# Kernel tuning notes

Hardware: AMD Instinct MI355X
Metric: run time of the kernel (lower is better)

The kernel has to match this reference:

```python
import jax, jax.numpy as jnp
import numpy as np

DIM = 1024
N_HIDDEN = 64
NUM_HEADS = 16
B, S = 4, 1024
# original torch code: scale = sqrt(n_hidden // num_heads) = sqrt(64 // 16) = 2.0
SCALE = float(np.sqrt(N_HIDDEN // NUM_HEADS))


def setup_inputs() -> dict:
    key = jax.random.key(0)
    ks = jax.random.split(key, 10)
    lim = 1.0 / np.sqrt(DIM)          # nn.Linear default init range
    lim_o = 1.0 / np.sqrt(N_HIDDEN * NUM_HEADS)
    u = lambda k, shape, l: jax.random.uniform(k, shape, jnp.float32, -l, l)
    x = jax.random.normal(ks[0], (B, S, DIM), jnp.float32)
    attn_mask = jax.random.randint(ks[1], (B, S, S), 0, 2).astype(jnp.int32)
    # stacked per-head projection weights: [H, dim, n_hidden]
    Wq = u(ks[2], (NUM_HEADS, DIM, N_HIDDEN), lim)
    bq = u(ks[3], (NUM_HEADS, N_HIDDEN), lim)
    Wk = u(ks[4], (NUM_HEADS, DIM, N_HIDDEN), lim)
    bk = u(ks[5], (NUM_HEADS, N_HIDDEN), lim)
    Wv = u(ks[6], (NUM_HEADS, DIM, N_HIDDEN), lim)
    bv = u(ks[7], (NUM_HEADS, N_HIDDEN), lim)
    Wo = u(ks[8], (NUM_HEADS * N_HIDDEN, DIM), lim_o)
    bo = u(ks[9], (DIM,), lim_o)
    return {"x": x, "attn_mask": attn_mask, "Wq": Wq, "bq": bq,
            "Wk": Wk, "bk": bk, "Wv": Wv, "bv": bv, "Wo": Wo, "bo": bo}


def reference(x, attn_mask, Wq, bq, Wk, bk, Wv, bv, Wo, bo):
    # batched QKV across all heads (replaces the per-head Python loop)
    Q = jnp.einsum('bsd,hde->bhse', x, Wq) + bq[None, :, None, :]
    K = jnp.einsum('bsd,hde->bhse', x, Wk) + bk[None, :, None, :]
    V = jnp.einsum('bsd,hde->bhse', x, Wv) + bv[None, :, None, :]
    scores = jnp.einsum('bhse,bhte->bhst', Q, K) / SCALE
    alpha = jax.nn.softmax(scores, axis=-1)
    # faithful to original: zero out masked entries AFTER softmax, no renorm
    alpha = jnp.where(attn_mask[:, None, :, :] == 0, 0.0, alpha)  # [B,H,S,S]
    out = jnp.einsum('bhst,bhte->bhse', alpha, V)                 # [B,H,S,E]
    # torch.cat over heads on last dim == reshape to [B,S,H*E] in head order
    concat = out.transpose(0, 2, 1, 3).reshape(B, S, NUM_HEADS * N_HIDDEN)
    attn_output = concat @ Wo + bo                                # [B,S,dim]
    return attn_output, alpha
```

## Files before the change

### kernel.cpp

```cpp
#include <hip/hip_runtime.h>
#include <stdint.h>

#define S_LEN 1024
#define DIM   1024
#define NHID  64
#define NHEAD 16
#define NB    4

typedef __bf16 bf16x8 __attribute__((ext_vector_type(8)));
typedef float  f32x4  __attribute__((ext_vector_type(4)));
typedef unsigned short u16;

__device__ __forceinline__ u16 f2b(float f) {
  unsigned u = __float_as_uint(f);
  u += 0x7FFFu + ((u >> 16) & 1u);
  return (u16)(u >> 16);
}

__device__ __forceinline__ f32x4 mfma16(bf16x8 a, bf16x8 b, f32x4 c) {
  return __builtin_amdgcn_mfma_f32_16x16x32_bf16(a, b, c, 0, 0, 0);
}

__global__ __launch_bounds__(256) void k_cvt_x(const float* __restrict__ x,
                                               u16* __restrict__ xb) {
  int i = blockIdx.x * 256 + threadIdx.x;
  float4 v = ((const float4*)x)[i];
  ushort4 o;
  o.x = f2b(v.x); o.y = f2b(v.y); o.z = f2b(v.z); o.w = f2b(v.w);
  ((ushort4*)xb)[i] = o;
}

__global__ __launch_bounds__(256) void k_maskbits(const int* __restrict__ mask,
                                                  uint32_t* __restrict__ bits) {
  int w = blockIdx.x * 256 + threadIdx.x;
  const int4* mp = (const int4*)mask + (size_t)w * 8;
  uint32_t v = 0;
#pragma unroll
  for (int i = 0; i < 8; ++i) {
    int4 m = mp[i];
    v |= (m.x != 0 ? 1u : 0u) << (i * 4 + 0);
    v |= (m.y != 0 ? 1u : 0u) << (i * 4 + 1);
    v |= (m.z != 0 ? 1u : 0u) << (i * 4 + 2);
    v |= (m.w != 0 ? 1u : 0u) << (i * 4 + 3);
  }
  bits[w] = v;
}

__global__ __launch_bounds__(256) void k_transpose(const float* __restrict__ in,
                                                   u16* __restrict__ out,
                                                   int R, int C) {
  const float* ip = in + (size_t)blockIdx.x * R * C;
  u16* op = out + (size_t)blockIdx.x * R * C;
  __shared__ float tile[32][65];
  int r0 = blockIdx.y * 32, c0 = blockIdx.z * 64;
  int t = threadIdx.x;
  {
    int col = t & 63, rr = t >> 6;
#pragma unroll
    for (int p = 0; p < 8; ++p) {
      int r = p * 4 + rr;
      tile[r][col] = ip[(size_t)(r0 + r) * C + c0 + col];
    }
  }
  __syncthreads();
  {
    int d = t & 31, er = t >> 5;
#pragma unroll
    for (int p = 0; p < 8; ++p) {
      int e = p * 8 + er;
      op[(size_t)(c0 + e) * R + r0 + d] = f2b(tile[d][e]);
    }
  }
}

__global__ __launch_bounds__(256) void k_qkv(const u16* __restrict__ xb,
                                             const u16* __restrict__ Wtb,
                                             const float* __restrict__ bq,
                                             const float* __restrict__ bk,
                                             const float* __restrict__ bv,
                                             u16* __restrict__ Qb,
                                             u16* __restrict__ Kb,
                                             u16* __restrict__ Vtb) {
  __shared__ __align__(16) char lds[32768];
  int t = threadIdx.x, w = t >> 6, lane = t & 63;
  int l15 = lane & 15, l4 = lane >> 4;
  int m0 = blockIdx.x * 128, n0 = blockIdx.y * 128, sel = blockIdx.z;
  const u16* Wh = Wtb + (size_t)sel * (NHEAD * NHID * DIM);
  int wr = w >> 1, wc = w & 1;

  f32x4 acc[4][4];
  const f32x4 fz = {0.f, 0.f, 0.f, 0.f};
#pragma unroll
  for (int i = 0; i < 4; ++i)
#pragma unroll
    for (int j = 0; j < 4; ++j) acc[i][j] = fz;

  for (int kk = 0; kk < 16; ++kk) {
    int k0 = kk * 64;
#pragma unroll
    for (int c = 0; c < 4; ++c) {
      int idx = c * 256 + t, r = idx >> 3, cb = idx & 7;
      int4 v = *(const int4*)(xb + (size_t)(m0 + r) * DIM + k0 + cb * 8);
      *(int4*)(lds + r * 128 + ((cb * 16) ^ ((r & 7) << 4))) = v;
    }
#pragma unroll
    for (int c = 0; c < 4; ++c) {
      int idx = c * 256 + t, r = idx >> 3, cb = idx & 7;
      int4 v = *(const int4*)(Wh + (size_t)(n0 + r) * DIM + k0 + cb * 8);
      *(int4*)(lds + 16384 + r * 128 + ((cb * 16) ^ ((r & 7) << 4))) = v;
    }
    __syncthreads();
    bf16x8 a[4][2], bb[4][2];
#pragma unroll
    for (int mf = 0; mf < 4; ++mf)
#pragma unroll
      for (int kc = 0; kc < 2; ++kc) {
        int row = wr * 64 + mf * 16 + l15;
        int kb = kc * 64 + l4 * 16;
        a[mf][kc] = *(const bf16x8*)(lds + row * 128 + (kb ^ ((row & 7) << 4)));
      }
#pragma unroll
    for (int nf = 0; nf < 4; ++nf)
#pragma unroll
      for (int kc = 0; kc < 2; ++kc) {
        int row = wc * 64 + nf * 16 + l15;
        int kb = kc * 64 + l4 * 16;
        bb[nf][kc] = *(const bf16x8*)(lds + 16384 + row * 128 + (kb ^ ((row & 7) << 4)));
      }
#pragma unroll
    for (int kc = 0; kc < 2; ++kc)
#pragma unroll
      for (int mf = 0; mf < 4; ++mf)
#pragma unroll
        for (int nf = 0; nf < 4; ++nf)
          acc[mf][nf] = mfma16(a[mf][kc], bb[nf][kc], acc[mf][nf]);
    __syncthreads();
  }

  const float* bias = (sel == 0) ? bq : (sel == 1) ? bk : bv;
  float postScale = (sel == 0) ? 0.5f : 1.0f;
#pragma unroll
  for (int nf = 0; nf < 4; ++nf) {
    int n = n0 + wc * 64 + nf * 16 + l15;
    int h = n >> 6, e = n & 63;
    float bv_ = bias[n];
#pragma unroll
    for (int mf = 0; mf < 4; ++mf) {
      int mrow0 = m0 + wr * 64 + mf * 16 + l4 * 4;
      int b_ = mrow0 >> 10, s0 = mrow0 & 1023;
      if (sel == 2) {
        ushort4 pk;
        pk.x = f2b(acc[mf][nf][0] + bv_);
        pk.y = f2b(acc[mf][nf][1] + bv_);
        pk.z = f2b(acc[mf][nf][2] + bv_);
        pk.w = f2b(acc[mf][nf][3] + bv_);
        *(ushort4*)(Vtb + ((size_t)(b_ * NHEAD + h) * NHID + e) * S_LEN + s0) = pk;
      } else {
        u16* dst = (sel == 0) ? Qb : Kb;
#pragma unroll
        for (int j = 0; j < 4; ++j)
          dst[((size_t)(b_ * NHEAD + h) * S_LEN + s0 + j) * NHID + e] =
              f2b((acc[mf][nf][j] + bv_) * postScale);
      }
    }
  }
}

__global__ __launch_bounds__(256, 4) void k_attn(const u16* __restrict__ Qb,
                                                 const u16* __restrict__ Kb,
                                                 const u16* __restrict__ Vtb,
                                                 const uint32_t* __restrict__ mbitsG,
                                                 float* __restrict__ alphaOut,
                                                 u16* __restrict__ Ob) {
  __shared__ __align__(16) char smem[19072];
  uint32_t* mbits = (uint32_t*)smem;
  float* redM = (float*)(smem + 2176);
  float* redS = (float*)(smem + 2432);
  char* chunkB = smem + 2688;
  int t = threadIdx.x, w = t >> 6, lane = t & 63;
  int l15 = lane & 15, l4 = lane >> 4;
  int q0 = blockIdx.x * 16;
  int bh = blockIdx.y, b = bh >> 4, hh = bh & 15;
  const u16* Qh = Qb + (size_t)bh * S_LEN * NHID;
  const u16* Kh = Kb + (size_t)bh * S_LEN * NHID;
  const u16* Vh = Vtb + (size_t)bh * NHID * S_LEN;
  int kbase = w * 256;

  uint2 mw2 = ((const uint2*)(mbitsG + ((size_t)b * S_LEN + q0) * 32))[t];

  bf16x8 aq[2];
#pragma unroll
  for (int ec = 0; ec < 2; ++ec)
    aq[ec] = *(const bf16x8*)(Qh + (size_t)(q0 + l15) * NHID + ec * 32 + l4 * 8);

  {
    int row = t >> 4, c0 = (t & 15) * 2;
    mbits[row * 33 + c0 + 0] = mw2.x;
    mbits[row * 33 + c0 + 1] = mw2.y;
  }

  f32x4 sc[16];
  const f32x4 fz = {0.f, 0.f, 0.f, 0.f};
#pragma unroll
  for (int kf = 0; kf < 16; ++kf) sc[kf] = fz;

#pragma unroll
  for (int kf = 0; kf < 16; ++kf) {
    int key = kbase + kf * 16 + l15;
    bf16x8 kb0 = *(const bf16x8*)(Kh + (size_t)key * NHID + l4 * 8);
    bf16x8 kb1 = *(const bf16x8*)(Kh + (size_t)key * NHID + 32 + l4 * 8);
    sc[kf] = mfma16(aq[0], kb0, sc[kf]);
    sc[kf] = mfma16(aq[1], kb1, sc[kf]);
  }

  float rm[4];
#pragma unroll
  for (int j = 0; j < 4; ++j) {
    float m = sc[0][j];
#pragma unroll
    for (int kf = 1; kf < 16; ++kf) m = fmaxf(m, sc[kf][j]);
    rm[j] = m;
  }
#pragma unroll
  for (int msk = 1; msk < 16; msk <<= 1)
#pragma unroll
    for (int j = 0; j < 4; ++j) rm[j] = fmaxf(rm[j], __shfl_xor(rm[j], msk));
  if (l15 == 0) {
#pragma unroll
    for (int j = 0; j < 4; ++j) redM[w * 16 + l4 * 4 + j] = rm[j];
  }
  __syncthreads();
  float Mx[4];
#pragma unroll
  for (int j = 0; j < 4; ++j) {
    int row = l4 * 4 + j;
    Mx[j] = fmaxf(fmaxf(redM[row], redM[16 + row]),
                  fmaxf(redM[32 + row], redM[48 + row]));
  }

  float ls[4] = {0.f, 0.f, 0.f, 0.f};
#pragma unroll
  for (int kf = 0; kf < 16; ++kf)
#pragma unroll
    for (int j = 0; j < 4; ++j) {
      float p = __expf(sc[kf][j] - Mx[j]);
      sc[kf][j] = p;
      ls[j] += p;
    }
#pragma unroll
  for (int msk = 1; msk < 16; msk <<= 1)
#pragma unroll
    for (int j = 0; j < 4; ++j) ls[j] += __shfl_xor(ls[j], msk);
  if (l15 == 0) {
#pragma unroll
    for (int j = 0; j < 4; ++j) redS[w * 16 + l4 * 4 + j] = ls[j];
  }
  __syncthreads();
  float inv[4];
#pragma unroll
  for (int j = 0; j < 4; ++j) {
    int row = l4 * 4 + j;
    inv[j] = 1.f / (redS[row] + redS[16 + row] + redS[32 + row] + redS[48 + row]);
  }

  float* abW = alphaOut + (size_t)bh * S_LEN * S_LEN;

  f32x4 o[4];
#pragma unroll
  for (int ef = 0; ef < 4; ++ef) o[ef] = fz;

  auto produce = [&](int c) {
    char* buf = chunkB + (w * 2 + (c & 1)) * 2048;
    int widxBase = w * 8 + c * 2;
#pragma unroll
    for (int f = 0; f < 4; ++f) {
      int kf = c * 4 + f;
      int keyg = kbase + kf * 16 + l15;
      int widx = widxBase + (f >> 1);
      int bitpos = ((f & 1) << 4) + l15;
#pragma unroll
      for (int j = 0; j < 4; ++j) {
        int row = l4 * 4 + j;
        uint32_t mwd = mbits[row * 33 + widx];
        float av = ((mwd >> bitpos) & 1u) ? sc[kf][j] * inv[j] : 0.f;
        __builtin_nontemporal_store(av, abW + (size_t)(q0 + row) * S_LEN + keyg);
        int klc = f * 16 + l15;
        *(u16*)(buf + row * 128 + ((2 * klc) ^ ((row & 7) << 4))) = f2b(av);
      }
    }
  };
  auto pv = [&](int c) {
    char* buf = chunkB + (w * 2 + (c & 1)) * 2048;
#pragma unroll
    for (int kc2 = 0; kc2 < 2; ++kc2) {
      int qrow = l15;
      bf16x8 pa = *(const bf16x8*)(buf + qrow * 128 +
                                   ((kc2 * 64 + l4 * 16) ^ ((qrow & 7) << 4)));
#pragma unroll
      for (int ef = 0; ef < 4; ++ef) {
        int e = ef * 16 + l15;
        bf16x8 vb = *(const bf16x8*)(Vh + (size_t)e * S_LEN + kbase + c * 64 +
                                     kc2 * 32 + l4 * 8);
        o[ef] = mfma16(pa, vb, o[ef]);
      }
    }
  };

  produce(0);
  produce(1); pv(0);
  produce(2); pv(1);
  produce(3); pv(2);
  pv(3);

  __syncthreads();
  float* redO = (float*)chunkB;
#pragma unroll
  for (int ef = 0; ef < 4; ++ef)
#pragma unroll
    for (int j = 0; j < 4; ++j)
      redO[w * 1024 + (l4 * 4 + j) * 64 + ef * 16 + l15] = o[ef][j];
  __syncthreads();
  {
    int e = t & 63, r4 = t >> 6;
#pragma unroll
    for (int p = 0; p < 4; ++p) {
      int r = p * 4 + r4;
      float s4 = redO[r * 64 + e] + redO[1024 + r * 64 + e] +
                 redO[2048 + r * 64 + e] + redO[3072 + r * 64 + e];
      Ob[(size_t)(b * S_LEN + q0 + r) * DIM + hh * NHID + e] = f2b(s4);
    }
  }
}

__global__ __launch_bounds__(256) void k_oproj(const u16* __restrict__ Ob,
                                               const u16* __restrict__ Wotb,
                                               const float* __restrict__ bo,
                                               float* __restrict__ out) {
  __shared__ __align__(16) char lds[32768];
  int t = threadIdx.x, w = t >> 6, lane = t & 63;
  int l15 = lane & 15, l4 = lane >> 4;
  int m0 = blockIdx.x * 128, n0 = blockIdx.y * 128;
  int wr = w >> 1, wc = w & 1;
  f32x4 acc[4][4];
  const f32x4 fz = {0.f, 0.f, 0.f, 0.f};
#pragma unroll
  for (int i = 0; i < 4; ++i)
#pragma unroll
    for (int j = 0; j < 4; ++j) acc[i][j] = fz;

  for (int kk = 0; kk < 16; ++kk) {
    int k0 = kk * 64;
#pragma unroll
    for (int c = 0; c < 4; ++c) {
      int idx = c * 256 + t, r = idx >> 3, cb = idx & 7;
      int4 v = *(const int4*)(Ob + (size_t)(m0 + r) * DIM + k0 + cb * 8);
      *(int4*)(lds + r * 128 + ((cb * 16) ^ ((r & 7) << 4))) = v;
    }
#pragma unroll
    for (int c = 0; c < 4; ++c) {
      int idx = c * 256 + t, r = idx >> 3, cb = idx & 7;
      int4 v = *(const int4*)(Wotb + (size_t)(n0 + r) * DIM + k0 + cb * 8);
      *(int4*)(lds + 16384 + r * 128 + ((cb * 16) ^ ((r & 7) << 4))) = v;
    }
    __syncthreads();
    bf16x8 a[4][2], bb[4][2];
#pragma unroll
    for (int mf = 0; mf < 4; ++mf)
#pragma unroll
      for (int kc = 0; kc < 2; ++kc) {
        int row = wr * 64 + mf * 16 + l15;
        int kb = kc * 64 + l4 * 16;
        a[mf][kc] = *(const bf16x8*)(lds + row * 128 + (kb ^ ((row & 7) << 4)));
      }
#pragma unroll
    for (int nf = 0; nf < 4; ++nf)
#pragma unroll
      for (int kc = 0; kc < 2; ++kc) {
        int row = wc * 64 + nf * 16 + l15;
        int kb = kc * 64 + l4 * 16;
        bb[nf][kc] = *(const bf16x8*)(lds + 16384 + row * 128 + (kb ^ ((row & 7) << 4)));
      }
#pragma unroll
    for (int kc = 0; kc < 2; ++kc)
#pragma unroll
      for (int mf = 0; mf < 4; ++mf)
#pragma unroll
        for (int nf = 0; nf < 4; ++nf)
          acc[mf][nf] = mfma16(a[mf][kc], bb[nf][kc], acc[mf][nf]);
    __syncthreads();
  }
#pragma unroll
  for (int nf = 0; nf < 4; ++nf) {
    int n = n0 + wc * 64 + nf * 16 + l15;
    float bv_ = bo[n];
#pragma unroll
    for (int mf = 0; mf < 4; ++mf)
#pragma unroll
      for (int j = 0; j < 4; ++j) {
        int m = m0 + wr * 64 + mf * 16 + l4 * 4 + j;
        out[(size_t)m * DIM + n] = acc[mf][nf][j] + bv_;
      }
  }
}

extern "C" void kernel_launch(void* const* d_in, const int* in_sizes, int n_in,
                              void* d_out, int out_size, void* d_ws, size_t ws_size,
                              hipStream_t stream) {
  const float* x    = (const float*)d_in[0];
  const int*   mask = (const int*)d_in[1];
  const float* Wq   = (const float*)d_in[2];
  const float* bq   = (const float*)d_in[3];
  const float* Wk   = (const float*)d_in[4];
  const float* bk   = (const float*)d_in[5];
  const float* Wv   = (const float*)d_in[6];
  const float* bv   = (const float*)d_in[7];
  const float* Wo   = (const float*)d_in[8];
  const float* bo   = (const float*)d_in[9];
  float* out = (float*)d_out;
  float* alphaOut = out + (size_t)NB * S_LEN * DIM;

  char* ws = (char*)d_ws;
  u16* xb    = (u16*)(ws);
  u16* Wtb   = (u16*)(ws + 8388608);
  u16* Wotb  = (u16*)(ws + 14680064);
  u16* Qb    = (u16*)(ws + 16777216);
  u16* Kb    = (u16*)(ws + 25165824);
  u16* Vtb   = (u16*)(ws + 33554432);
  u16* Ob    = (u16*)(ws + 41943040);
  uint32_t* mbits = (uint32_t*)(ws + 50331648);

  k_maskbits<<<512, 256, 0, stream>>>(mask, mbits);
  k_cvt_x<<<4096, 256, 0, stream>>>(x, xb);
  k_transpose<<<dim3(16, 32, 1), 256, 0, stream>>>(Wq, Wtb,           1024, 64);
  k_transpose<<<dim3(16, 32, 1), 256, 0, stream>>>(Wk, Wtb + 1048576, 1024, 64);
  k_transpose<<<dim3(16, 32, 1), 256, 0, stream>>>(Wv, Wtb + 2097152, 1024, 64);
  k_transpose<<<dim3(1, 32, 16), 256, 0, stream>>>(Wo, Wotb,          1024, 1024);
  k_qkv<<<dim3(32, 8, 3), 256, 0, stream>>>(xb, Wtb, bq, bk, bv, Qb, Kb, Vtb);
  k_attn<<<dim3(64, 64), 256, 0, stream>>>(Qb, Kb, Vtb, mbits, alphaOut, Ob);
  k_oproj<<<dim3(32, 8), 256, 0, stream>>>(Ob, Wotb, bo, out);
}
```

Measured before the change: 226.1 us.

## Transpose QK^T MFMA so each lane owns one query row for vectorized alpha stores

Swaps the MFMA operand order so the score tile is transposed and each lane holds four consecutive keys of a single query row. The alpha output can then be written as one 16-byte nontemporal store per fragment instead of scalar stores, and the bf16 P tile goes to LDS as packed 8-byte writes. Row max and sum reductions shrink to two cross-lane shuffles on one scalar, and mask words are read directly from global into registers, removing the mask LDS staging. The cost is a switch-based selection of the mask word and a changed LDS layout for the P buffer, which must still match the PV reader's swizzle.

```diff
diff --git a/kernel.cpp b/kernel.cpp
--- a/kernel.cpp
+++ b/kernel.cpp
@@ -172,11 +172,10 @@
                                                  const uint32_t* __restrict__ mbitsG,
                                                  float* __restrict__ alphaOut,
                                                  u16* __restrict__ Ob) {
-  __shared__ __align__(16) char smem[19072];
-  uint32_t* mbits = (uint32_t*)smem;
-  float* redM = (float*)(smem + 2176);
-  float* redS = (float*)(smem + 2432);
-  char* chunkB = smem + 2688;
+  __shared__ __align__(16) char smem[16896];
+  float* redM = (float*)(smem + 16384);
+  float* redS = (float*)(smem + 16640);
+  char* chunkB = smem;
   int t = threadIdx.x, w = t >> 6, lane = t & 63;
   int l15 = lane & 15, l4 = lane >> 4;
   int q0 = blockIdx.x * 16;
@@ -186,18 +185,14 @@
   const u16* Vh = Vtb + (size_t)bh * NHID * S_LEN;
   int kbase = w * 256;
 
-  uint2 mw2 = ((const uint2*)(mbitsG + ((size_t)b * S_LEN + q0) * 32))[t];
+  const uint32_t* mrow = mbitsG + ((size_t)b * S_LEN + q0 + l15) * 32 + w * 8;
+  uint4 mw0 = *(const uint4*)(mrow);
+  uint4 mw1 = *(const uint4*)(mrow + 4);
 
   bf16x8 aq[2];
 #pragma unroll
   for (int ec = 0; ec < 2; ++ec)
     aq[ec] = *(const bf16x8*)(Qh + (size_t)(q0 + l15) * NHID + ec * 32 + l4 * 8);
-
-  {
-    int row = t >> 4, c0 = (t & 15) * 2;
-    mbits[row * 33 + c0 + 0] = mw2.x;
-    mbits[row * 33 + c0 + 1] = mw2.y;
-  }
 
   f32x4 sc[16];
   const f32x4 fz = {0.f, 0.f, 0.f, 0.f};
@@ -209,59 +204,46 @@
     int key = kbase + kf * 16 + l15;
     bf16x8 kb0 = *(const bf16x8*)(Kh + (size_t)key * NHID + l4 * 8);
     bf16x8 kb1 = *(const bf16x8*)(Kh + (size_t)key * NHID + 32 + l4 * 8);
-    sc[kf] = mfma16(aq[0], kb0, sc[kf]);
-    sc[kf] = mfma16(aq[1], kb1, sc[kf]);
-  }
-
-  float rm[4];
-#pragma unroll
-  for (int j = 0; j < 4; ++j) {
-    float m = sc[0][j];
-#pragma unroll
-    for (int kf = 1; kf < 16; ++kf) m = fmaxf(m, sc[kf][j]);
-    rm[j] = m;
-  }
-#pragma unroll
-  for (int msk = 1; msk < 16; msk <<= 1)
-#pragma unroll
-    for (int j = 0; j < 4; ++j) rm[j] = fmaxf(rm[j], __shfl_xor(rm[j], msk));
-  if (l15 == 0) {
-#pragma unroll
-    for (int j = 0; j < 4; ++j) redM[w * 16 + l4 * 4 + j] = rm[j];
-  }
+    sc[kf] = mfma16(kb0, aq[0], sc[kf]);
+    sc[kf] = mfma16(kb1, aq[1], sc[kf]);
+  }
+
+  float m;
+  {
+    f32x4 mm = sc[0];
+#pragma unroll
+    for (int kf = 1; kf < 16; ++kf) {
+      mm[0] = fmaxf(mm[0], sc[kf][0]);
+      mm[1] = fmaxf(mm[1], sc[kf][1]);
+      mm[2] = fmaxf(mm[2], sc[kf][2]);
+      mm[3] = fmaxf(mm[3], sc[kf][3]);
+    }
+    m = fmaxf(fmaxf(mm[0], mm[1]), fmaxf(mm[2], mm[3]));
+  }
+  m = fmaxf(m, __shfl_xor(m, 16));
+  m = fmaxf(m, __shfl_xor(m, 32));
+  if (lane < 16) redM[w * 16 + l15] = m;
   __syncthreads();
-  float Mx[4];
-#pragma unroll
-  for (int j = 0; j < 4; ++j) {
-    int row = l4 * 4 + j;
-    Mx[j] = fmaxf(fmaxf(redM[row], redM[16 + row]),
-                  fmaxf(redM[32 + row], redM[48 + row]));
-  }
-
-  float ls[4] = {0.f, 0.f, 0.f, 0.f};
-#pragma unroll
-  for (int kf = 0; kf < 16; ++kf)
-#pragma unroll
-    for (int j = 0; j < 4; ++j) {
-      float p = __expf(sc[kf][j] - Mx[j]);
-      sc[kf][j] = p;
-      ls[j] += p;
-    }
-#pragma unroll
-  for (int msk = 1; msk < 16; msk <<= 1)
-#pragma unroll
-    for (int j = 0; j < 4; ++j) ls[j] += __shfl_xor(ls[j], msk);
-  if (l15 == 0) {
-#pragma unroll
-    for (int j = 0; j < 4; ++j) redS[w * 16 + l4 * 4 + j] = ls[j];
-  }
+  float Mx = fmaxf(fmaxf(redM[l15], redM[16 + l15]),
+                   fmaxf(redM[32 + l15], redM[48 + l15]));
+
+  float s0 = 0.f, s1 = 0.f, s2 = 0.f, s3 = 0.f;
+#pragma unroll
+  for (int kf = 0; kf < 16; ++kf) {
+    f32x4 p;
+    p[0] = __expf(sc[kf][0] - Mx);
+    p[1] = __expf(sc[kf][1] - Mx);
+    p[2] = __expf(sc[kf][2] - Mx);
+    p[3] = __expf(sc[kf][3] - Mx);
+    sc[kf] = p;
+    s0 += p[0]; s1 += p[1]; s2 += p[2]; s3 += p[3];
+  }
+  float ls = (s0 + s1) + (s2 + s3);
+  ls += __shfl_xor(ls, 16);
+  ls += __shfl_xor(ls, 32);
+  if (lane < 16) redS[w * 16 + l15] = ls;
   __syncthreads();
-  float inv[4];
-#pragma unroll
-  for (int j = 0; j < 4; ++j) {
-    int row = l4 * 4 + j;
-    inv[j] = 1.f / (redS[row] + redS[16 + row] + redS[32 + row] + redS[48 + row]);
-  }
+  float inv = 1.f / (redS[l15] + redS[16 + l15] + redS[32 + l15] + redS[48 + l15]);
 
   float* abW = alphaOut + (size_t)bh * S_LEN * S_LEN;
 
@@ -271,22 +253,33 @@
 
   auto produce = [&](int c) {
     char* buf = chunkB + (w * 2 + (c & 1)) * 2048;
-    int widxBase = w * 8 + c * 2;
 #pragma unroll
     for (int f = 0; f < 4; ++f) {
       int kf = c * 4 + f;
-      int keyg = kbase + kf * 16 + l15;
-      int widx = widxBase + (f >> 1);
-      int bitpos = ((f & 1) << 4) + l15;
-#pragma unroll
-      for (int j = 0; j < 4; ++j) {
-        int row = l4 * 4 + j;
-        uint32_t mwd = mbits[row * 33 + widx];
-        float av = ((mwd >> bitpos) & 1u) ? sc[kf][j] * inv[j] : 0.f;
-        __builtin_nontemporal_store(av, abW + (size_t)(q0 + row) * S_LEN + keyg);
-        int klc = f * 16 + l15;
-        *(u16*)(buf + row * 128 + ((2 * klc) ^ ((row & 7) << 4))) = f2b(av);
-      }
+      int wi = kf >> 1;
+      uint32_t mword;
+      switch (wi) {
+        case 0: mword = mw0.x; break;
+        case 1: mword = mw0.y; break;
+        case 2: mword = mw0.z; break;
+        case 3: mword = mw0.w; break;
+        case 4: mword = mw1.x; break;
+        case 5: mword = mw1.y; break;
+        case 6: mword = mw1.z; break;
+        default: mword = mw1.w; break;
+      }
+      int bbase = ((kf & 1) << 4) + l4 * 4;
+      f32x4 av;
+      av[0] = ((mword >> (bbase + 0)) & 1u) ? sc[kf][0] * inv : 0.f;
+      av[1] = ((mword >> (bbase + 1)) & 1u) ? sc[kf][1] * inv : 0.f;
+      av[2] = ((mword >> (bbase + 2)) & 1u) ? sc[kf][2] * inv : 0.f;
+      av[3] = ((mword >> (bbase + 3)) & 1u) ? sc[kf][3] * inv : 0.f;
+      __builtin_nontemporal_store(
+          av, (f32x4*)(abW + (size_t)(q0 + l15) * S_LEN + kbase + kf * 16 + l4 * 4));
+      uint32_t p01 = (uint32_t)f2b(av[0]) | ((uint32_t)f2b(av[1]) << 16);
+      uint32_t p23 = (uint32_t)f2b(av[2]) | ((uint32_t)f2b(av[3]) << 16);
+      uint2 pk; pk.x = p01; pk.y = p23;
+      *(uint2*)(buf + l15 * 128 + ((f * 32 + l4 * 8) ^ ((l15 & 7) << 4))) = pk;
     }
   };
   auto pv = [&](int c) {
```

New measurement: 242.5 us. +7.3%, slower.
